# Optimization experiments

Hardware: AMD Instinct MI355X
Metric: run time of the kernel (lower is better)

## Reference

```python
import jax, jax.numpy as jnp
import numpy as np

S = 8            # num_subgroups
BLUR = 1e-4      # sinkhorn_blur
P_NORM = 2       # sinkhorn_p -> cost = |x-y|^2 / 2, eps = blur**2
SCALING = 0.9    # geomloss scaling -> eps ratio = scaling**2


def _eps_schedule(eps0, eps_target, ratio):
    # static (trace-time) epsilon-scaling schedule, geomloss-style
    eps_list = []
    eps = eps0
    while eps > eps_target:
        eps_list.append(eps)
        eps *= ratio
    eps_list.append(eps_target)
    return np.asarray(eps_list, dtype=np.float32)


def _softmin(eps, C, h):
    # -eps * log sum_j (1/m) exp((h_j - C_ij)/eps); C: [...,n,m], h: [...,m] -> [...,n]
    m = C.shape[-1]
    return -eps * (jax.nn.logsumexp((h[..., None, :] - C) / eps, axis=-1) - jnp.log(m))


def _sqcost(X, Y):
    # 0.5 * squared euclidean distance; [...,n,d] x [...,m,d] -> [...,n,m]
    xx = jnp.sum(X * X, axis=-1)[..., :, None]
    yy = jnp.sum(Y * Y, axis=-1)[..., None, :]
    xy = jnp.einsum('...nd,...md->...nm', X, Y)
    return 0.5 * jnp.maximum(xx + yy - 2.0 * xy, 0.0)


def setup_inputs() -> dict:
    key = jax.random.key(0)
    B, D = 8192, 256
    features = jax.random.normal(key, (B, D), dtype=jnp.float32)
    # balanced subgroup labels so every subgroup has exactly B//S samples
    subgroups = (jnp.arange(B) % S).astype(jnp.int32)
    return {"features": features, "subgroups": subgroups}


def reference(features, subgroups):
    B, D = features.shape
    n = B // S                                   # samples per subgroup (balanced)
    order = jnp.argsort(subgroups, stable=True)  # group rows, preserving in-group order
    G = features[order].reshape(S, n, D)         # [S, n, D]

    ii, jj = np.triu_indices(S, 1)               # 28 subgroup pairs (static)
    Xi, Xj = G[ii], G[jj]                        # [P, n, D]
    Cxy = _sqcost(Xi, Xj)                        # [P, n, n] cross costs
    Cxx = _sqcost(G, G)                          # [S, n, n] self costs (debiasing)
    Cxy_d = jax.lax.stop_gradient(Cxy)
    Cxx_d = jax.lax.stop_gradient(Cxx)

    eps_target = BLUR ** P_NORM
    eps_sched = jnp.asarray(_eps_schedule(float(D), eps_target, SCALING ** P_NORM))

    P = Cxy.shape[0]
    f0 = jnp.zeros((P, n), jnp.float32)
    g0 = jnp.zeros((P, n), jnp.float32)
    s0 = jnp.zeros((S, n), jnp.float32)

    def step(carry, eps):
        f, g, s = carry
        ft = _softmin(eps, Cxy_d, g)                       # Jacobi update x<-y
        gt = _softmin(eps, jnp.swapaxes(Cxy_d, -1, -2), f) # Jacobi update y<-x
        st = 0.5 * (s + _softmin(eps, Cxx_d, s))           # symmetric self update
        return (ft, gt, st), None

    (f, g, s), _ = jax.lax.scan(step, (f0, g0, s0), eps_sched)

    # final extrapolation through the differentiable cost (geomloss-style grads)
    f_fin = _softmin(eps_target, Cxy, jax.lax.stop_gradient(g))
    g_fin = _softmin(eps_target, jnp.swapaxes(Cxy, -1, -2), jax.lax.stop_gradient(f))
    s_fin = _softmin(eps_target, Cxx, jax.lax.stop_gradient(s))

    # debiased Sinkhorn divergence per pair: <a, f - p_x> + <b, g - p_y>
    pair_losses = jnp.mean(f_fin - s_fin[ii], axis=-1) + jnp.mean(g_fin - s_fin[jj], axis=-1)
    total_loss = jnp.mean(pair_losses)
    return total_loss, pair_losses
```

## Files before the change

kernel.cpp:

```cpp
#include <hip/hip_runtime.h>
#include <hip/hip_fp16.h>
#include <cstddef>
#include <cstdint>

#define NSG   8
#define NPAIR 28
#define NBLK  36
#define NPT   1024
#define DIM   256
#define NROW  8192
#define LOG_N  6.9314718055994531f
#define LOG2E  1.4426950408889634f

__constant__ int c_pa[NBLK] = {0,0,0,0,0,0,0,1,1,1,1,1,1,2,2,2,2,2,3,3,3,3,4,4,4,5,5,6, 0,1,2,3,4,5,6,7};
__constant__ int c_pb[NBLK] = {1,2,3,4,5,6,7,2,3,4,5,6,7,3,4,5,6,7,4,5,6,7,5,6,7,6,7,7, 0,1,2,3,4,5,6,7};

__device__ __forceinline__ float wredMax(float v) {
#pragma unroll
  for (int o = 32; o > 0; o >>= 1) v = fmaxf(v, __shfl_xor(v, o, 64));
  return v;
}
__device__ __forceinline__ float wredMin(float v) {
#pragma unroll
  for (int o = 32; o > 0; o >>= 1) v = fminf(v, __shfl_xor(v, o, 64));
  return v;
}
__device__ __forceinline__ float wredSum(float v) {
#pragma unroll
  for (int o = 32; o > 0; o >>= 1) v += __shfl_xor(v, o, 64);
  return v;
}

__device__ __forceinline__ void cvt16(float4 A, float4 B, float* c) {
  const __half2* ha = (const __half2*)&A;
  const __half2* hb = (const __half2*)&B;
#pragma unroll
  for (int i = 0; i < 4; i++) {
    float2 f = __half22float2(ha[i]);
    c[2 * i] = f.x; c[2 * i + 1] = f.y;
  }
#pragma unroll
  for (int i = 0; i < 4; i++) {
    float2 f = __half22float2(hb[i]);
    c[8 + 2 * i] = f.x; c[8 + 2 * i + 1] = f.y;
  }
}

__device__ __forceinline__ float ub(unsigned int w, int s) {
  return (float)((w >> s) & 0xffu);
}

__global__ void build_idx(const int* __restrict__ sg, int* __restrict__ idx, int* __restrict__ cnt) {
  int i = blockIdx.x * 256 + threadIdx.x;
  if (i >= NROW) return;
  int s = sg[i];
  int r = atomicAdd(&cnt[s], 1);
  idx[s * NPT + r] = i;
}

__global__ void gather_rows(const float* __restrict__ feat, const int* __restrict__ idx,
                            float* __restrict__ G, float* __restrict__ sq) {
  int row = blockIdx.x;
  int src = idx[row];
  float v = feat[(size_t)src * DIM + threadIdx.x];
  G[(size_t)row * DIM + threadIdx.x] = v;
  float p = wredSum(v * v);
  __shared__ float ws[4];
  if ((threadIdx.x & 63) == 0) ws[threadIdx.x >> 6] = p;
  __syncthreads();
  if (threadIdx.x == 0) sq[row] = 0.5f * (ws[0] + ws[1] + ws[2] + ws[3]);
}

__global__ __launch_bounds__(256) void cost_gemm(const float* __restrict__ G,
                                                 const float* __restrict__ sq,
                                                 __half* __restrict__ Ch) {
  __shared__ float As[8][128];
  __shared__ float Bt[8][128];
  int blk = blockIdx.x;
  int b = blk >> 6, t = blk & 63;
  int sa = c_pa[b], sb = c_pb[b];
  int i0 = (t >> 3) << 7, j0 = (t & 7) << 7;
  const float* Arows = G + (size_t)(sa * NPT + i0) * DIM;
  const float* Brows = G + (size_t)(sb * NPT + j0) * DIM;
  int tid = threadIdx.x;
  int ty = tid >> 4, tx = tid & 15;
  float acc[8][8];
#pragma unroll
  for (int r = 0; r < 8; r++)
#pragma unroll
    for (int q = 0; q < 8; q++) acc[r][q] = 0.f;

  int lrow = tid >> 1, lk4 = (tid & 1) << 2;
  for (int k0 = 0; k0 < DIM; k0 += 8) {
    __syncthreads();
    float4 av = *(const float4*)(Arows + (size_t)lrow * DIM + k0 + lk4);
    float4 bv = *(const float4*)(Brows + (size_t)lrow * DIM + k0 + lk4);
    As[lk4 + 0][lrow] = av.x; As[lk4 + 1][lrow] = av.y; As[lk4 + 2][lrow] = av.z; As[lk4 + 3][lrow] = av.w;
    Bt[lk4 + 0][lrow] = bv.x; Bt[lk4 + 1][lrow] = bv.y; Bt[lk4 + 2][lrow] = bv.z; Bt[lk4 + 3][lrow] = bv.w;
    __syncthreads();
#pragma unroll
    for (int kk = 0; kk < 8; kk++) {
      float4 a0 = *(const float4*)&As[kk][ty << 3];
      float4 a1 = *(const float4*)&As[kk][(ty << 3) + 4];
      float4 b0 = *(const float4*)&Bt[kk][tx << 3];
      float4 b1 = *(const float4*)&Bt[kk][(tx << 3) + 4];
      float ar[8] = {a0.x, a0.y, a0.z, a0.w, a1.x, a1.y, a1.z, a1.w};
      float br[8] = {b0.x, b0.y, b0.z, b0.w, b1.x, b1.y, b1.z, b1.w};
#pragma unroll
      for (int r = 0; r < 8; r++)
#pragma unroll
        for (int q = 0; q < 8; q++) acc[r][q] = fmaf(ar[r], br[q], acc[r][q]);
    }
  }
  __half* dst = Ch + ((size_t)b << 20);
  float sqa[8], sqb[8];
#pragma unroll
  for (int r = 0; r < 8; r++) sqa[r] = sq[sa * NPT + i0 + (ty << 3) + r];
#pragma unroll
  for (int q = 0; q < 8; q++) sqb[q] = sq[sb * NPT + j0 + (tx << 3) + q];
#pragma unroll
  for (int r = 0; r < 8; r++) {
    __half* drow = dst + (size_t)(i0 + (ty << 3) + r) * NPT + j0 + (tx << 3);
    union { float4 f4; __half h[8]; } o;
#pragma unroll
    for (int q = 0; q < 8; q++)
      o.h[q] = __float2half_rn(fmaxf(sqa[r] + sqb[q] - acc[r][q], 0.f));
    *(float4*)drow = o.f4;
  }
}

__global__ __launch_bounds__(256) void quant_row(const __half* __restrict__ Ch,
                                                 unsigned char* __restrict__ C8,
                                                 float2* __restrict__ rowScale) {
  const int blk = blockIdx.x;
  const int b = blk >> 4, rowblk = blk & 15;
  const int sa = c_pa[b], sb = c_pb[b];
  const int q = (sa == sb) ? 9 * sa : 8 * sa + sb;
  const __half* src = Ch + ((size_t)b << 20);
  unsigned char* dst = C8 + ((size_t)q << 20);
  const int wave = threadIdx.x >> 6, lane = threadIdx.x & 63;
  for (int jj = 0; jj < 16; jj++) {
    const int row = (rowblk << 6) + (jj << 2) + wave;
    const float4* s4 = (const float4*)(src + ((size_t)row << 10) + (lane << 4));
    float c[16];
    cvt16(s4[0], s4[1], c);
    float mn = c[0], mx = c[0];
#pragma unroll
    for (int t = 1; t < 16; t++) { mn = fminf(mn, c[t]); mx = fmaxf(mx, c[t]); }
    mn = wredMin(mn);
    mx = wredMax(mx);
    const float range = mx - mn;
    const float scale = (range > 1e-6f) ? range * (1.0f / 255.0f) : 1.0f;
    const float inv = (range > 1e-6f) ? 255.0f / range : 0.0f;
    unsigned int w[4];
#pragma unroll
    for (int d = 0; d < 4; d++) {
      unsigned int u0 = min(__float2uint_rn((c[4 * d + 0] - mn) * inv), 255u);
      unsigned int u1 = min(__float2uint_rn((c[4 * d + 1] - mn) * inv), 255u);
      unsigned int u2 = min(__float2uint_rn((c[4 * d + 2] - mn) * inv), 255u);
      unsigned int u3 = min(__float2uint_rn((c[4 * d + 3] - mn) * inv), 255u);
      w[d] = u0 | (u1 << 8) | (u2 << 16) | (u3 << 24);
    }
    *(uint4*)(dst + ((size_t)row << 10) + (lane << 4)) = make_uint4(w[0], w[1], w[2], w[3]);
    if (lane == 0) rowScale[(q << 10) + row] = make_float2(mn, scale);
  }
}

__global__ __launch_bounds__(256) void colminmax(const __half* __restrict__ Ch,
                                                 float4* __restrict__ pMn, float4* __restrict__ pMx) {
  const int blk = blockIdx.x;
  const int p = blk >> 3, rb = blk & 7;
  const int j0 = threadIdx.x << 2;
  const __half* src = Ch + ((size_t)p << 20) + j0;
  float mn[4] = {3.4e38f, 3.4e38f, 3.4e38f, 3.4e38f};
  float mx[4] = {-3.4e38f, -3.4e38f, -3.4e38f, -3.4e38f};
  for (int r = 0; r < 128; r++) {
    const int row = (rb << 7) + r;
    uint2 raw = *(const uint2*)(src + ((size_t)row << 10));
    const __half2* hh = (const __half2*)&raw;
    float2 f0 = __half22float2(hh[0]);
    float2 f1 = __half22float2(hh[1]);
    float v[4] = {f0.x, f0.y, f1.x, f1.y};
#pragma unroll
    for (int t = 0; t < 4; t++) { mn[t] = fminf(mn[t], v[t]); mx[t] = fmaxf(mx[t], v[t]); }
  }
  const int o = ((p << 3) + rb) * 256 + threadIdx.x;
  pMn[o] = make_float4(mn[0], mn[1], mn[2], mn[3]);
  pMx[o] = make_float4(mx[0], mx[1], mx[2], mx[3]);
}

__global__ void colreduce(const float4* __restrict__ pMn, const float4* __restrict__ pMx,
                          float2* __restrict__ rowScale) {
  const int id = blockIdx.x * 256 + threadIdx.x;
  const int p = id >> 8, t = id & 255;
  float4 mn = pMn[(p << 3) * 256 + t];
  float4 mx = pMx[(p << 3) * 256 + t];
  for (int rb = 1; rb < 8; rb++) {
    float4 a = pMn[((p << 3) + rb) * 256 + t];
    float4 b = pMx[((p << 3) + rb) * 256 + t];
    mn.x = fminf(mn.x, a.x); mn.y = fminf(mn.y, a.y); mn.z = fminf(mn.z, a.z); mn.w = fminf(mn.w, a.w);
    mx.x = fmaxf(mx.x, b.x); mx.y = fmaxf(mx.y, b.y); mx.z = fmaxf(mx.z, b.z); mx.w = fmaxf(mx.w, b.w);
  }
  const int qT = 8 * c_pb[p] + c_pa[p];
  float bs[4] = {mn.x, mn.y, mn.z, mn.w};
  float xs[4] = {mx.x, mx.y, mx.z, mx.w};
#pragma unroll
  for (int cc = 0; cc < 4; cc++) {
    float range = xs[cc] - bs[cc];
    float scale = (range > 1e-6f) ? range * (1.0f / 255.0f) : 1.0f;
    rowScale[(qT << 10) + (t << 2) + cc] = make_float2(bs[cc], scale);
  }
}

__global__ __launch_bounds__(256) void quantT(const __half* __restrict__ Ch,
                                              const float2* __restrict__ rowScale,
                                              unsigned char* __restrict__ C8) {
  __shared__ __half t[64][72];
  const int blk = blockIdx.x;
  const int p = blk >> 8, tb = blk & 255;
  const int i0 = (tb >> 4) << 6, j0 = (tb & 15) << 6;
  const int qT = 8 * c_pb[p] + c_pa[p];
  const __half* src = Ch + ((size_t)p << 20);
  unsigned char* dst = C8 + ((size_t)qT << 20);
  const int tid = threadIdx.x;
  const int r = tid >> 2, cg = (tid & 3) << 4;
  const float4* s4 = (const float4*)(src + ((size_t)(i0 + r) << 10) + j0 + cg);
  float4 v0 = s4[0], v1 = s4[1];
  *(float4*)&t[r][cg] = v0;
  *(float4*)&t[r][cg + 8] = v1;
  __syncthreads();
  const int jr = j0 + r;
  const float2 sc = rowScale[(qT << 10) + jr];
  const float inv = 1.0f / sc.y;
  unsigned int w[4];
#pragma unroll
  for (int d = 0; d < 4; d++) {
    unsigned int uu[4];
#pragma unroll
    for (int e = 0; e < 4; e++) {
      float c = __half2float(t[cg + 4 * d + e][r]);
      uu[e] = min(__float2uint_rn((c - sc.x) * inv), 255u);
    }
    w[d] = uu[0] | (uu[1] << 8) | (uu[2] << 16) | (uu[3] << 24);
  }
  *(uint4*)(dst + ((size_t)jr << 10) + i0 + cg) = make_uint4(w[0], w[1], w[2], w[3]);
}

template <bool LSE>
__global__ __launch_bounds__(256) void sink_step(
    const unsigned char* __restrict__ C8, const float2* __restrict__ rowScale,
    const float* __restrict__ pot_cur, float* __restrict__ pot_nxt,
    float eps, float csS, float cmS) {
  const int i = blockIdx.x;
  const int x = i & 7, rr = i >> 3;
  const int q = ((rr & 7) << 3) | x;
  const int chunk = rr >> 3;
  const int mate = ((q & 7) << 3) | (q >> 3);
  const bool diag = (mate == q);
  const float cs = diag ? csS : 0.f;
  const float cm = diag ? cmS : 1.f;
  const int wave = threadIdx.x >> 6, lane = threadIdx.x & 63;
  const float* hp = pot_cur + (mate << 10) + (lane << 4);
  float h[16];
  {
    float4 h0 = ((const float4*)hp)[0], h1 = ((const float4*)hp)[1];
    float4 h2 = ((const float4*)hp)[2], h3 = ((const float4*)hp)[3];
    h[0]=h0.x; h[1]=h0.y; h[2]=h0.z; h[3]=h0.w;
    h[4]=h1.x; h[5]=h1.y; h[6]=h1.z; h[7]=h1.w;
    h[8]=h2.x; h[9]=h2.y; h[10]=h2.z; h[11]=h2.w;
    h[12]=h3.x; h[13]=h3.y; h[14]=h3.z; h[15]=h3.w;
  }
  const float c0 = LOG2E / eps;
  const unsigned char* Cb = C8 + ((size_t)q << 20) + ((size_t)chunk << 15) + (lane << 4);

  uint4 uv[8];
#pragma unroll
  for (int k = 0; k < 8; k++)
    uv[k] = *(const uint4*)(Cb + ((size_t)((k << 2) + wave) << 10));

#pragma unroll
  for (int k = 0; k < 8; k++) {
    const int row = (chunk << 5) + (k << 2) + wave;
    const float2 rs = rowScale[(q << 10) + row];
    const float ns = -rs.y;
    float a[16];
#pragma unroll
    for (int d = 0; d < 4; d++) {
      const unsigned int w = (&uv[k].x)[d];
      a[4 * d + 0] = fmaf(ub(w, 0),  ns, h[4 * d + 0] - rs.x);
      a[4 * d + 1] = fmaf(ub(w, 8),  ns, h[4 * d + 1] - rs.x);
      a[4 * d + 2] = fmaf(ub(w, 16), ns, h[4 * d + 2] - rs.x);
      a[4 * d + 3] = fmaf(ub(w, 24), ns, h[4 * d + 3] - rs.x);
    }
    float m = a[0];
#pragma unroll
    for (int t = 1; t < 16; t++) m = fmaxf(m, a[t]);
    m = wredMax(m);
    float sm;
    if (LSE) {
      float ss = 0.f;
#pragma unroll
      for (int t = 0; t < 16; t++) ss += exp2f((a[t] - m) * c0);
      ss = wredSum(ss);
      sm = -(m + eps * (__logf(ss) - LOG_N));
    } else {
      sm = -m;
    }
    if (lane == 0)
      pot_nxt[(q << 10) + row] = cs * pot_cur[(q << 10) + row] + cm * sm;
  }
}

__global__ void loss_pairs(const float* __restrict__ pot, float* __restrict__ out) {
  int pb = blockIdx.x;
  int si = c_pa[pb], sj = c_pb[pb];
  const float* fv = pot + ((8 * si + sj) << 10);
  const float* gv = pot + ((8 * sj + si) << 10);
  const float* sa = pot + ((9 * si) << 10);
  const float* sb = pot + ((9 * sj) << 10);
  float acc = 0.f;
  for (int t = threadIdx.x; t < NPT; t += 256)
    acc += (fv[t] - sa[t]) + (gv[t] - sb[t]);
  acc = wredSum(acc);
  __shared__ float wsm[4];
  if ((threadIdx.x & 63) == 0) wsm[threadIdx.x >> 6] = acc;
  __syncthreads();
  if (threadIdx.x == 0) out[1 + pb] = (wsm[0] + wsm[1] + wsm[2] + wsm[3]) * (1.0f / NPT);
}

__global__ void loss_total(float* __restrict__ out) {
  int t = threadIdx.x;
  float x = (t < NPAIR) ? out[1 + t] : 0.f;
  x = wredSum(x);
  if (t == 0) out[0] = x / (float)NPAIR;
}

extern "C" void kernel_launch(void* const* d_in, const int* in_sizes, int n_in,
                              void* d_out, int out_size, void* d_ws, size_t ws_size,
                              hipStream_t stream) {
  const float* feat = (const float*)d_in[0];
  const int* sg = (const int*)d_in[1];
  float* out = (float*)d_out;
  char* ws = (char*)d_ws;

  size_t o = 0;
  __half* Ch = (__half*)(ws + o); o += (size_t)NBLK * NPT * NPT * 2;
  unsigned char* C8 = (unsigned char*)(ws + o); o += (size_t)64 * NPT * NPT;
  float2* rowScale = (float2*)(ws + o); o += (size_t)64 * NPT * 8;
  float4* pMn = (float4*)(ws + o); o += (size_t)NPAIR * 8 * 256 * 16;
  float4* pMx = (float4*)(ws + o); o += (size_t)NPAIR * 8 * 256 * 16;
  float* G  = (float*)(ws + o); o += (size_t)NROW * DIM * 4;
  float* sq = (float*)(ws + o); o += (size_t)NROW * 4;
  int* idx  = (int*)(ws + o); o += (size_t)NROW * 4;
  int* cnt  = (int*)(ws + o); o += 1024;
  float* pot[2];
  pot[0] = (float*)(ws + o); o += (size_t)64 * NPT * 4;
  pot[1] = (float*)(ws + o); o += (size_t)64 * NPT * 4;

  hipMemsetAsync(cnt, 0, 1024, stream);
  hipMemsetAsync(pot[0], 0, (size_t)64 * NPT * 4, stream);

  build_idx<<<NROW / 256, 256, 0, stream>>>(sg, idx, cnt);
  gather_rows<<<NROW, 256, 0, stream>>>(feat, idx, G, sq);
  cost_gemm<<<NBLK * 64, 256, 0, stream>>>(G, sq, Ch);
  quant_row<<<NBLK * 16, 256, 0, stream>>>(Ch, C8, rowScale);
  colminmax<<<NPAIR * 8, 256, 0, stream>>>(Ch, pMn, pMx);
  colreduce<<<NPAIR, 256, 0, stream>>>(pMn, pMx, rowScale);
  quantT<<<NPAIR * 256, 256, 0, stream>>>(Ch, rowScale, C8);

  float sched[256];
  int ns = 0;
  {
    double e = 256.0;
    const double ratio = 0.9 * 0.9;
    const double tgt = 1e-4 * 1e-4;
    while (e > tgt) { sched[ns++] = (float)e; e *= ratio; }
    sched[ns++] = (float)tgt;
  }
  const float epsT = sched[ns - 1];
  const float EPS_CUT = 1e-3f;

  int cur = 0;
  for (int k = 0; k < ns; k++) {
    if (sched[k] >= EPS_CUT)
      sink_step<true><<<64 * 32, 256, 0, stream>>>(C8, rowScale, pot[cur], pot[1 - cur],
                                                   sched[k], 0.5f, 0.5f);
    else
      sink_step<false><<<64 * 32, 256, 0, stream>>>(C8, rowScale, pot[cur], pot[1 - cur],
                                                    sched[k], 0.5f, 0.5f);
    cur ^= 1;
  }
  sink_step<false><<<64 * 32, 256, 0, stream>>>(C8, rowScale, pot[cur], pot[1 - cur],
                                                epsT, 0.0f, 1.0f);
  cur ^= 1;
  loss_pairs<<<NPAIR, 256, 0, stream>>>(pot[cur], out);
  loss_total<<<1, 64, 0, stream>>>(out);
}
```

Baseline: 3.230 ms.

## Move cost GEMM to bf16 MFMA and streamline Sinkhorn step arithmetic

The gathered features are now stored as bf16, and the fp32 FMA cost GEMM is replaced by a bf16 MFMA 16x16x32 kernel that fills shared memory through direct global-to-LDS loads. The Sinkhorn step pre-scales the potentials by log2e/eps so the exp2 needs no extra multiply. It also splits the row loads into two halves to lower register pressure and raises the occupancy launch bound. Storing inputs in bf16 loses precision in the cross term of the cost, which could affect accuracy at small eps.

```diff
diff --git a/kernel.cpp b/kernel.cpp
--- a/kernel.cpp
+++ b/kernel.cpp
@@ -11,6 +11,11 @@
 #define NROW  8192
 #define LOG_N  6.9314718055994531f
 #define LOG2E  1.4426950408889634f
+#define LN2    0.69314718055994531f
+
+typedef unsigned short u16;
+typedef __attribute__((ext_vector_type(8))) short bfrag;
+typedef __attribute__((ext_vector_type(4))) float f32x4;
 
 __constant__ int c_pa[NBLK] = {0,0,0,0,0,0,0,1,1,1,1,1,1,2,2,2,2,2,3,3,3,3,4,4,4,5,5,6, 0,1,2,3,4,5,6,7};
 __constant__ int c_pb[NBLK] = {1,2,3,4,5,6,7,2,3,4,5,6,7,3,4,5,6,7,4,5,6,7,5,6,7,6,7,7, 0,1,2,3,4,5,6,7};
@@ -48,6 +53,11 @@
 
 __device__ __forceinline__ float ub(unsigned int w, int s) {
   return (float)((w >> s) & 0xffu);
+}
+
+__device__ __forceinline__ void gload_lds16(const void* g, void* l) {
+  __builtin_amdgcn_global_load_lds((const __attribute__((address_space(1))) void*)g,
+                                   (__attribute__((address_space(3))) void*)l, 16, 0, 0);
 }
 
 __global__ void build_idx(const int* __restrict__ sg, int* __restrict__ idx, int* __restrict__ cnt) {
@@ -59,11 +69,13 @@
 }
 
 __global__ void gather_rows(const float* __restrict__ feat, const int* __restrict__ idx,
-                            float* __restrict__ G, float* __restrict__ sq) {
+                            u16* __restrict__ Gh, float* __restrict__ sq) {
   int row = blockIdx.x;
   int src = idx[row];
   float v = feat[(size_t)src * DIM + threadIdx.x];
-  G[(size_t)row * DIM + threadIdx.x] = v;
+  unsigned int u = __float_as_uint(v);
+  unsigned int r = (u + 0x7fffu + ((u >> 16) & 1u)) >> 16;
+  Gh[(size_t)row * DIM + threadIdx.x] = (u16)r;
   float p = wredSum(v * v);
   __shared__ float ws[4];
   if ((threadIdx.x & 63) == 0) ws[threadIdx.x >> 6] = p;
@@ -71,61 +83,80 @@
   if (threadIdx.x == 0) sq[row] = 0.5f * (ws[0] + ws[1] + ws[2] + ws[3]);
 }
 
-__global__ __launch_bounds__(256) void cost_gemm(const float* __restrict__ G,
+__global__ __launch_bounds__(256) void cost_gemm(const u16* __restrict__ Gh,
                                                  const float* __restrict__ sq,
                                                  __half* __restrict__ Ch) {
-  __shared__ float As[8][128];
-  __shared__ float Bt[8][128];
-  int blk = blockIdx.x;
-  int b = blk >> 6, t = blk & 63;
-  int sa = c_pa[b], sb = c_pb[b];
-  int i0 = (t >> 3) << 7, j0 = (t & 7) << 7;
-  const float* Arows = G + (size_t)(sa * NPT + i0) * DIM;
-  const float* Brows = G + (size_t)(sb * NPT + j0) * DIM;
-  int tid = threadIdx.x;
-  int ty = tid >> 4, tx = tid & 15;
-  float acc[8][8];
-#pragma unroll
-  for (int r = 0; r < 8; r++)
-#pragma unroll
-    for (int q = 0; q < 8; q++) acc[r][q] = 0.f;
-
-  int lrow = tid >> 1, lk4 = (tid & 1) << 2;
-  for (int k0 = 0; k0 < DIM; k0 += 8) {
+  __shared__ __align__(16) u16 As[4][128][8];
+  __shared__ __align__(16) u16 Bs[4][128][8];
+  const int blk = blockIdx.x;
+  const int b = blk >> 6, t = blk & 63;
+  const int sa = c_pa[b], sb = c_pb[b];
+  const int i0 = (t >> 3) << 7, j0 = (t & 7) << 7;
+  const int tid = threadIdx.x;
+  const int lane = tid & 63;
+  const int wid = tid >> 6;
+  const int wr = wid >> 1, wc = wid & 1;
+  const int kq = lane >> 4, r16 = lane & 15;
+
+  const u16* Abase = Gh + (size_t)(sa * NPT + i0) * DIM;
+  const u16* Bbase = Gh + (size_t)(sb * NPT + j0) * DIM;
+
+  const int su0 = tid, su1 = 256 + tid;
+  const int sg0 = su0 >> 7, sr0 = su0 & 127;
+  const int sg1 = su1 >> 7, sr1 = su1 & 127;
+
+  f32x4 acc[4][4];
+#pragma unroll
+  for (int mi = 0; mi < 4; mi++)
+#pragma unroll
+    for (int nj = 0; nj < 4; nj++) {
+      f32x4 z = {0.f, 0.f, 0.f, 0.f};
+      acc[mi][nj] = z;
+    }
+
+  for (int k0 = 0; k0 < DIM; k0 += 32) {
     __syncthreads();
-    float4 av = *(const float4*)(Arows + (size_t)lrow * DIM + k0 + lk4);
-    float4 bv = *(const float4*)(Brows + (size_t)lrow * DIM + k0 + lk4);
-    As[lk4 + 0][lrow] = av.x; As[lk4 + 1][lrow] = av.y; As[lk4 + 2][lrow] = av.z; As[lk4 + 3][lrow] = av.w;
-    Bt[lk4 + 0][lrow] = bv.x; Bt[lk4 + 1][lrow] = bv.y; Bt[lk4 + 2][lrow] = bv.z; Bt[lk4 + 3][lrow] = bv.w;
+    gload_lds16(Abase + (size_t)sr0 * DIM + k0 + sg0 * 8, (char*)As + su0 * 16);
+    gload_lds16(Abase + (size_t)sr1 * DIM + k0 + sg1 * 8, (char*)As + su1 * 16);
+    gload_lds16(Bbase + (size_t)sr0 * DIM + k0 + sg0 * 8, (char*)Bs + su0 * 16);
+    gload_lds16(Bbase + (size_t)sr1 * DIM + k0 + sg1 * 8, (char*)Bs + su1 * 16);
     __syncthreads();
-#pragma unroll
-    for (int kk = 0; kk < 8; kk++) {
-      float4 a0 = *(const float4*)&As[kk][ty << 3];
-      float4 a1 = *(const float4*)&As[kk][(ty << 3) + 4];
-      float4 b0 = *(const float4*)&Bt[kk][tx << 3];
-      float4 b1 = *(const float4*)&Bt[kk][(tx << 3) + 4];
-      float ar[8] = {a0.x, a0.y, a0.z, a0.w, a1.x, a1.y, a1.z, a1.w};
-      float br[8] = {b0.x, b0.y, b0.z, b0.w, b1.x, b1.y, b1.z, b1.w};
-#pragma unroll
-      for (int r = 0; r < 8; r++)
-#pragma unroll
-        for (int q = 0; q < 8; q++) acc[r][q] = fmaf(ar[r], br[q], acc[r][q]);
+    bfrag af[4], bf[4];
+#pragma unroll
+    for (int mi = 0; mi < 4; mi++)
+      af[mi] = *(const bfrag*)&As[kq][wr * 64 + mi * 16 + r16][0];
+#pragma unroll
+    for (int nj = 0; nj < 4; nj++)
+      bf[nj] = *(const bfrag*)&Bs[kq][wc * 64 + nj * 16 + r16][0];
+#pragma unroll
+    for (int mi = 0; mi < 4; mi++)
+#pragma unroll
+      for (int nj = 0; nj < 4; nj++)
+        acc[mi][nj] = __builtin_amdgcn_mfma_f32_16x16x32_bf16(af[mi], bf[nj], acc[mi][nj], 0, 0, 0);
+  }
+
+  float4 sqa[4];
+#pragma unroll
+  for (int mi = 0; mi < 4; mi++)
+    sqa[mi] = *(const float4*)&sq[sa * NPT + i0 + wr * 64 + mi * 16 + 4 * kq];
+  float sqb[4];
+#pragma unroll
+  for (int nj = 0; nj < 4; nj++)
+    sqb[nj] = sq[sb * NPT + j0 + wc * 64 + nj * 16 + r16];
+  __half* dst = Ch + ((size_t)b << 20);
+#pragma unroll
+  for (int mi = 0; mi < 4; mi++) {
+    const int rowb = i0 + wr * 64 + mi * 16 + 4 * kq;
+#pragma unroll
+    for (int r = 0; r < 4; r++) {
+      const float sav = ((const float*)&sqa[mi])[r];
+      __half* drow = dst + ((size_t)(rowb + r) << 10);
+#pragma unroll
+      for (int nj = 0; nj < 4; nj++) {
+        const int col = j0 + wc * 64 + nj * 16 + r16;
+        drow[col] = __float2half_rn(fmaxf(sav + sqb[nj] - acc[mi][nj][r], 0.f));
+      }
     }
-  }
-  __half* dst = Ch + ((size_t)b << 20);
-  float sqa[8], sqb[8];
-#pragma unroll
-  for (int r = 0; r < 8; r++) sqa[r] = sq[sa * NPT + i0 + (ty << 3) + r];
-#pragma unroll
-  for (int q = 0; q < 8; q++) sqb[q] = sq[sb * NPT + j0 + (tx << 3) + q];
-#pragma unroll
-  for (int r = 0; r < 8; r++) {
-    __half* drow = dst + (size_t)(i0 + (ty << 3) + r) * NPT + j0 + (tx << 3);
-    union { float4 f4; __half h[8]; } o;
-#pragma unroll
-    for (int q = 0; q < 8; q++)
-      o.h[q] = __float2half_rn(fmaxf(sqa[r] + sqb[q] - acc[r][q], 0.f));
-    *(float4*)drow = o.f4;
   }
 }
 
@@ -247,7 +278,7 @@
 }
 
 template <bool LSE>
-__global__ __launch_bounds__(256) void sink_step(
+__global__ __launch_bounds__(256, 8) void sink_step(
     const unsigned char* __restrict__ C8, const float2* __restrict__ rowScale,
     const float* __restrict__ pot_cur, float* __restrict__ pot_nxt,
     float eps, float csS, float cmS) {
@@ -260,54 +291,62 @@
   const float cs = diag ? csS : 0.f;
   const float cm = diag ? cmS : 1.f;
   const int wave = threadIdx.x >> 6, lane = threadIdx.x & 63;
-  const float* hp = pot_cur + (mate << 10) + (lane << 4);
+  const float c0 = LOG2E / eps;
+  const float el2 = eps * LN2;
   float h[16];
   {
-    float4 h0 = ((const float4*)hp)[0], h1 = ((const float4*)hp)[1];
-    float4 h2 = ((const float4*)hp)[2], h3 = ((const float4*)hp)[3];
+    const float4* hp = (const float4*)(pot_cur + (mate << 10) + (lane << 4));
+    float4 h0 = hp[0], h1 = hp[1], h2 = hp[2], h3 = hp[3];
     h[0]=h0.x; h[1]=h0.y; h[2]=h0.z; h[3]=h0.w;
     h[4]=h1.x; h[5]=h1.y; h[6]=h1.z; h[7]=h1.w;
     h[8]=h2.x; h[9]=h2.y; h[10]=h2.z; h[11]=h2.w;
     h[12]=h3.x; h[13]=h3.y; h[14]=h3.z; h[15]=h3.w;
   }
-  const float c0 = LOG2E / eps;
+  if (LSE) {
+#pragma unroll
+    for (int tt = 0; tt < 16; tt++) h[tt] *= c0;
+  }
   const unsigned char* Cb = C8 + ((size_t)q << 20) + ((size_t)chunk << 15) + (lane << 4);
-
-  uint4 uv[8];
-#pragma unroll
-  for (int k = 0; k < 8; k++)
-    uv[k] = *(const uint4*)(Cb + ((size_t)((k << 2) + wave) << 10));
-
-#pragma unroll
-  for (int k = 0; k < 8; k++) {
-    const int row = (chunk << 5) + (k << 2) + wave;
-    const float2 rs = rowScale[(q << 10) + row];
-    const float ns = -rs.y;
-    float a[16];
-#pragma unroll
-    for (int d = 0; d < 4; d++) {
-      const unsigned int w = (&uv[k].x)[d];
-      a[4 * d + 0] = fmaf(ub(w, 0),  ns, h[4 * d + 0] - rs.x);
-      a[4 * d + 1] = fmaf(ub(w, 8),  ns, h[4 * d + 1] - rs.x);
-      a[4 * d + 2] = fmaf(ub(w, 16), ns, h[4 * d + 2] - rs.x);
-      a[4 * d + 3] = fmaf(ub(w, 24), ns, h[4 * d + 3] - rs.x);
+  const int rb = chunk << 5;
+
+#pragma unroll
+  for (int half = 0; half < 2; half++) {
+    uint4 uv[4];
+#pragma unroll
+    for (int k = 0; k < 4; k++)
+      uv[k] = *(const uint4*)(Cb + ((size_t)((half << 4) + (k << 2) + wave) << 10));
+#pragma unroll
+    for (int k = 0; k < 4; k++) {
+      const int row = rb + (half << 4) + (k << 2) + wave;
+      const float2 rs = rowScale[(q << 10) + row];
+      const float ns = LSE ? (-rs.y) * c0 : -rs.y;
+      const unsigned int w0 = uv[k].x, w1 = uv[k].y, w2 = uv[k].z, w3 = uv[k].w;
+      float b[16];
+      b[0]  = fmaf(ub(w0, 0),  ns, h[0]);  b[1]  = fmaf(ub(w0, 8),  ns, h[1]);
+      b[2]  = fmaf(ub(w0, 16), ns, h[2]);  b[3]  = fmaf(ub(w0, 24), ns, h[3]);
+      b[4]  = fmaf(ub(w1, 0),  ns, h[4]);  b[5]  = fmaf(ub(w1, 8),  ns, h[5]);
+      b[6]  = fmaf(ub(w1, 16), ns, h[6]);  b[7]  = fmaf(ub(w1, 24), ns, h[7]);
+      b[8]  = fmaf(ub(w2, 0),  ns, h[8]);  b[9]  = fmaf(ub(w2, 8),  ns, h[9]);
+      b[10] = fmaf(ub(w2, 16), ns, h[10]); b[11] = fmaf(ub(w2, 24), ns, h[11]);
+      b[12] = fmaf(ub(w3, 0),  ns, h[12]); b[13] = fmaf(ub(w3, 8),  ns, h[13]);
+      b[14] = fmaf(ub(w3, 16), ns, h[14]); b[15] = fmaf(ub(w3, 24), ns, h[15]);
+      float m = b[0];
+#pragma unroll
+      for (int tt = 1; tt < 16; tt++) m = fmaxf(m, b[tt]);
+      m = wredMax(m);
+      float sm;
+      if (LSE) {
+        float ss = 0.f;
+#pragma unroll
+        for (int tt = 0; tt < 16; tt++) ss += exp2f(b[tt] - m);
+        ss = wredSum(ss);
+        sm = rs.x - fmaf(el2, m, eps * (__logf(ss) - LOG_N));
+      } else {
+        sm = rs.x - m;
+      }
+      if (lane == 0)
+        pot_nxt[(q << 10) + row] = cs * pot_cur[(q << 10) + row] + cm * sm;
     }
-    float m = a[0];
-#pragma unroll
-    for (int t = 1; t < 16; t++) m = fmaxf(m, a[t]);
-    m = wredMax(m);
-    float sm;
-    if (LSE) {
-      float ss = 0.f;
-#pragma unroll
-      for (int t = 0; t < 16; t++) ss += exp2f((a[t] - m) * c0);
-      ss = wredSum(ss);
-      sm = -(m + eps * (__logf(ss) - LOG_N));
-    } else {
-      sm = -m;
-    }
-    if (lane == 0)
-      pot_nxt[(q << 10) + row] = cs * pot_cur[(q << 10) + row] + cm * sm;
   }
 }
 
@@ -349,7 +388,7 @@
   float2* rowScale = (float2*)(ws + o); o += (size_t)64 * NPT * 8;
   float4* pMn = (float4*)(ws + o); o += (size_t)NPAIR * 8 * 256 * 16;
   float4* pMx = (float4*)(ws + o); o += (size_t)NPAIR * 8 * 256 * 16;
-  float* G  = (float*)(ws + o); o += (size_t)NROW * DIM * 4;
+  u16* Gh  = (u16*)(ws + o); o += (size_t)NROW * DIM * 2;
   float* sq = (float*)(ws + o); o += (size_t)NROW * 4;
   int* idx  = (int*)(ws + o); o += (size_t)NROW * 4;
   int* cnt  = (int*)(ws + o); o += 1024;
@@ -361,8 +400,8 @@
   hipMemsetAsync(pot[0], 0, (size_t)64 * NPT * 4, stream);
 
   build_idx<<<NROW / 256, 256, 0, stream>>>(sg, idx, cnt);
-  gather_rows<<<NROW, 256, 0, stream>>>(feat, idx, G, sq);
-  cost_gemm<<<NBLK * 64, 256, 0, stream>>>(G, sq, Ch);
+  gather_rows<<<NROW, 256, 0, stream>>>(feat, idx, Gh, sq);
+  cost_gemm<<<NBLK * 64, 256, 0, stream>>>(Gh, sq, Ch);
   quant_row<<<NBLK * 16, 256, 0, stream>>>(Ch, C8, rowScale);
   colminmax<<<NPAIR * 8, 256, 0, stream>>>(Ch, pMn, pMx);
   colreduce<<<NPAIR, 256, 0, stream>>>(pMn, pMx, rowScale);
```

Measured after the change: 2.653 ms. 17.9% less time.
